# Performance work log

Measured on AMD Instinct MI355X. Metric: run time of the kernel, lower is better.

The kernel has to match this reference:

```python
import jax, jax.numpy as jnp
import numpy as np

GRID_SIZE = 8
IN_DIM = 1024
OUT_DIM = 1024
BATCH = 4096


def setup_inputs() -> dict:
    key = jax.random.key(0)
    k1, k2, k3 = jax.random.split(key, 3)
    noise_scale = 0.1
    noise_scale_base = 0.1
    x = jax.random.normal(k1, (BATCH, IN_DIM), dtype=jnp.float32)
    scale_base = (1.0 / np.sqrt(IN_DIM)
                  + (jax.random.normal(k2, (OUT_DIM, IN_DIM), dtype=jnp.float32) * 2 - 1)
                  * noise_scale_base)
    scale_spline = jnp.full((OUT_DIM, IN_DIM), 1.0, dtype=jnp.float32)
    coeff = (jax.random.uniform(k3, (2, OUT_DIM, IN_DIM, GRID_SIZE), dtype=jnp.float32)
             * noise_scale / (np.sqrt(IN_DIM) * np.sqrt(GRID_SIZE)))
    return {"x": x, "scale_base": scale_base, "scale_spline": scale_spline,
            "coeff": coeff}


def reference(x, scale_base, scale_spline, coeff):
    # x: (B, I); scale_base/scale_spline: (O, I); coeff: (2, O, I, G)
    G = coeff.shape[-1]
    k = jnp.arange(1, G + 1, dtype=x.dtype)          # (G,)
    ang = x[:, :, None] * k                           # (B, I, G)
    cos_b = jnp.cos(ang)
    sin_b = jnp.sin(ang)
    # fold scale_spline into coeff: (2, O, I, G)
    w = scale_spline[None, :, :, None] * coeff
    spline = (jnp.einsum('big,oig->bo', cos_b, w[0])
              + jnp.einsum('big,oig->bo', sin_b, w[1]))  # (B, O)
    base = jnp.einsum('bi,oi->bo', jax.nn.silu(x), scale_base)
    return base + spline
```

## Files before the change

### kernel.cpp

```cpp
#include <hip/hip_runtime.h>
#include <hip/hip_bf16.h>
#include <stdint.h>

#define BATCH   4096
#define IN_DIM  1024
#define OUT_DIM 1024
#define GRID_G  8
#define K8      16384
#define KB      1024
#define SPLITK  2
#define WSCALE  256.0f

typedef __bf16 bf16x8 __attribute__((ext_vector_type(8)));
typedef __bf16 bf16x4 __attribute__((ext_vector_type(4)));
typedef float  f32x4  __attribute__((ext_vector_type(4)));
typedef int    i32x4  __attribute__((ext_vector_type(4)));
typedef int    i32x8  __attribute__((ext_vector_type(8)));

__global__ __launch_bounds__(256) void prep(const float* __restrict__ x,
                                            const float* __restrict__ sb,
                                            const float* __restrict__ ss,
                                            const float* __restrict__ coeff,
                                            uint8_t* __restrict__ A8,
                                            uint8_t* __restrict__ W8,
                                            __bf16* __restrict__ Ab,
                                            __bf16* __restrict__ Wb,
                                            float* __restrict__ C) {
    __shared__ __align__(16) float lds[8192];
    const int tid = threadIdx.x;

    if (blockIdx.x < 1024) {
        const int t  = blockIdx.x * 256 + tid;
        const int b  = t >> 6;
        const int i0 = (t & 63) * 16;

        {
            float4 z = make_float4(0.f, 0.f, 0.f, 0.f);
            float4* cz = (float4*)(C + (size_t)blockIdx.x * 4096);
#pragma unroll
            for (int j = 0; j < 4; ++j) cz[j * 256 + tid] = z;
        }

        float xv[16];
        {
            const f32x4* xp = (const f32x4*)(x + (size_t)b * IN_DIM + i0);
            f32x4 q0 = __builtin_nontemporal_load(xp + 0);
            f32x4 q1 = __builtin_nontemporal_load(xp + 1);
            f32x4 q2 = __builtin_nontemporal_load(xp + 2);
            f32x4 q3 = __builtin_nontemporal_load(xp + 3);
#pragma unroll
            for (int j = 0; j < 4; ++j) {
                xv[j]      = q0[j];
                xv[4 + j]  = q1[j];
                xv[8 + j]  = q2[j];
                xv[12 + j] = q3[j];
            }
        }

        float c1[16], s1[16], ck[16], sk[16];
        bf16x8 va, vb;
#pragma unroll
        for (int j = 0; j < 16; ++j) {
            float e  = __expf(-xv[j]);
            float sl = xv[j] * __builtin_amdgcn_rcpf(1.f + e);
            if (j < 8) va[j & 7] = (__bf16)sl; else vb[j & 7] = (__bf16)sl;
            s1[j] = __sinf(xv[j]);
            c1[j] = __cosf(xv[j]);
            ck[j] = c1[j]; sk[j] = s1[j];
        }
        __builtin_nontemporal_store(va, (bf16x8*)(Ab + (size_t)b * IN_DIM + i0));
        __builtin_nontemporal_store(vb, (bf16x8*)(Ab + (size_t)b * IN_DIM + i0 + 8));

        uint8_t* a8 = A8 + (size_t)b * K8 + i0;
#pragma unroll
        for (int g = 0; g < GRID_G; ++g) {
            i32x4 wc, ws;
#pragma unroll
            for (int q = 0; q < 4; ++q) {
                int dc = 0, ds = 0;
                dc = __builtin_amdgcn_cvt_pk_fp8_f32(ck[4*q+0], ck[4*q+1], dc, false);
                dc = __builtin_amdgcn_cvt_pk_fp8_f32(ck[4*q+2], ck[4*q+3], dc, true);
                ds = __builtin_amdgcn_cvt_pk_fp8_f32(sk[4*q+0], sk[4*q+1], ds, false);
                ds = __builtin_amdgcn_cvt_pk_fp8_f32(sk[4*q+2], sk[4*q+3], ds, true);
                wc[q] = dc; ws[q] = ds;
            }
            __builtin_nontemporal_store(wc, (i32x4*)(a8 + (size_t)g * IN_DIM));
            __builtin_nontemporal_store(ws, (i32x4*)(a8 + (size_t)(GRID_G + g) * IN_DIM));
            if (g < GRID_G - 1) {
#pragma unroll
                for (int j = 0; j < 16; ++j) {
                    float cn = ck[j] * c1[j] - sk[j] * s1[j];
                    float sn = sk[j] * c1[j] + ck[j] * s1[j];
                    ck[j] = cn; sk[j] = sn;
                }
            }
        }
    } else {
        const int o   = blockIdx.x - 1024;
        const int i0  = tid * 4;
        const size_t oi = (size_t)o * IN_DIM + i0;

        const f32x4 s4 = __builtin_nontemporal_load((const f32x4*)(ss + oi));
        const float  s[4] = {s4[0] * WSCALE, s4[1] * WSCALE, s4[2] * WSCALE, s4[3] * WSCALE};

        {
            f32x4 b4 = __builtin_nontemporal_load((const f32x4*)(sb + oi));
            bf16x4 wv;
            wv[0] = (__bf16)b4[0]; wv[1] = (__bf16)b4[1];
            wv[2] = (__bf16)b4[2]; wv[3] = (__bf16)b4[3];
            __builtin_nontemporal_store(wv, (bf16x4*)(Wb + oi));
        }

        uint8_t* w8 = W8 + (size_t)o * K8 + i0;
        for (int p = 0; p < 2; ++p) {
            if (p) __syncthreads();
            const f32x4* src = (const f32x4*)(coeff + ((size_t)p * OUT_DIM + o) * (IN_DIM * GRID_G));
#pragma unroll
            for (int j = 0; j < 8; ++j) {
                f32x4 v = __builtin_nontemporal_load(src + j * 256 + tid);
                const int L   = j * 4096 + tid * 16;
                const int row = L >> 7;
                const int ch  = (L >> 4) & 7;
                *(f32x4*)((uint8_t*)lds + row * 128 + ((ch ^ (row & 7)) << 4)) = v;
            }
            __syncthreads();
            float c[4][8];
            {
                const uint8_t* rp = (const uint8_t*)lds + tid * 128;
                const int r7 = (tid & 7) << 4;
#pragma unroll
                for (int j = 0; j < 8; ++j) {
                    f32x4 v = *(const f32x4*)(rp + ((j << 4) ^ r7));
                    c[j >> 1][(j & 1) * 4 + 0] = v[0];
                    c[j >> 1][(j & 1) * 4 + 1] = v[1];
                    c[j >> 1][(j & 1) * 4 + 2] = v[2];
                    c[j >> 1][(j & 1) * 4 + 3] = v[3];
                }
            }
#pragma unroll
            for (int g = 0; g < GRID_G; ++g) {
                int d = 0;
                d = __builtin_amdgcn_cvt_pk_fp8_f32(s[0]*c[0][g], s[1]*c[1][g], d, false);
                d = __builtin_amdgcn_cvt_pk_fp8_f32(s[2]*c[2][g], s[3]*c[3][g], d, true);
                __builtin_nontemporal_store(d, (int*)(w8 + (size_t)(p * GRID_G + g) * IN_DIM));
            }
        }
    }
}

__global__ __launch_bounds__(256, 2) void gemm_all(const uint8_t* __restrict__ A8,
                                                   const uint8_t* __restrict__ W8,
                                                   const uint8_t* __restrict__ Ab,
                                                   const uint8_t* __restrict__ Wb,
                                                   float* __restrict__ C) {
    __shared__ __align__(16) uint8_t As[2][16384];
    __shared__ __align__(16) uint8_t Bs[2][16384];
    const int tid = threadIdx.x;
    const int w   = tid >> 6;
    const int l   = tid & 63;
    const int flat = blockIdx.y * 8 + blockIdx.x;
    const int xcd  = flat & 7;
    const int idx  = flat >> 3;
    const int bn   = (xcd & 1) * 4 + (idx & 3);
    const int bm   = (xcd >> 1) * 8 + (idx >> 2);
    const int kz  = blockIdx.z;
    const int wm  = w & 1;
    const int wn  = w >> 1;

    f32x4 acc[4][4] = {};

    const int srow   = l >> 3;
    const int schunk = ((l & 7) ^ srow) * 16;
    const int lm = l & 15;
    const int q  = l >> 4;
    const int c0 = (q * 2) << 4, c1 = (q * 2 + 1) << 4;

    {
        const uint8_t* Ag = A8 + (size_t)(bm * 128 + w * 32 + srow) * K8 + kz * (K8 / SPLITK) + schunk;
        const uint8_t* Bg = W8 + (size_t)(bn * 128 + w * 32 + srow) * K8 + kz * (K8 / SPLITK) + schunk;

        auto stage = [&](int bb) {
#pragma unroll
            for (int j = 0; j < 4; ++j) {
                __builtin_amdgcn_global_load_lds(
                    (const uint32_t*)(Ag + (size_t)(j * 8) * K8),
                    (uint32_t*)(&As[bb][(w * 32 + j * 8) * 128]), 16, 0, 0);
                __builtin_amdgcn_global_load_lds(
                    (const uint32_t*)(Bg + (size_t)(j * 8) * K8),
                    (uint32_t*)(&Bs[bb][(w * 32 + j * 8) * 128]), 16, 0, 0);
            }
            Ag += 128; Bg += 128;
        };
        auto compute = [&](int bb) {
            i32x8 bf[4];
#pragma unroll
            for (int j = 0; j < 4; ++j) {
                const int row = wn * 64 + j * 16 + lm;
                const int sw  = (row & 7) << 4;
                const uint8_t* rp = &Bs[bb][row * 128];
                i32x4 lo = *(const i32x4*)(rp + (c0 ^ sw));
                i32x4 hi = *(const i32x4*)(rp + (c1 ^ sw));
                bf[j] = __builtin_shufflevector(lo, hi, 0, 1, 2, 3, 4, 5, 6, 7);
            }
#pragma unroll
            for (int i = 0; i < 4; ++i) {
                const int row = wm * 64 + i * 16 + lm;
                const int sw  = (row & 7) << 4;
                const uint8_t* rp = &As[bb][row * 128];
                i32x4 lo = *(const i32x4*)(rp + (c0 ^ sw));
                i32x4 hi = *(const i32x4*)(rp + (c1 ^ sw));
                i32x8 af = __builtin_shufflevector(lo, hi, 0, 1, 2, 3, 4, 5, 6, 7);
#pragma unroll
                for (int j = 0; j < 4; ++j)
                    acc[i][j] = __builtin_amdgcn_mfma_scale_f32_16x16x128_f8f6f4(
                        af, bf[j], acc[i][j], 0, 0, 0, 0x7f7f7f7f, 0, 0x7f7f7f7f);
            }
        };

        stage(0);
        __syncthreads();
        for (int ks = 0; ks < 32; ++ks) {
            stage(1);
            compute(0);
            __syncthreads();
            if (ks < 31) stage(0);
            compute(1);
            __syncthreads();
        }
    }

#pragma unroll
    for (int i = 0; i < 4; ++i)
#pragma unroll
        for (int j = 0; j < 4; ++j)
            acc[i][j] *= (1.0f / WSCALE);

    {
        const uint8_t* Ag = Ab + (size_t)(bm * 128 + w * 32 + srow) * (KB * 2) + kz * (KB * 2 / SPLITK) + schunk;
        const uint8_t* Bg = Wb + (size_t)(bn * 128 + w * 32 + srow) * (KB * 2) + kz * (KB * 2 / SPLITK) + schunk;

        auto stage = [&](int bb) {
#pragma unroll
            for (int j = 0; j < 4; ++j) {
                __builtin_amdgcn_global_load_lds(
                    (const uint32_t*)(Ag + (size_t)(j * 8) * (KB * 2)),
                    (uint32_t*)(&As[bb][(w * 32 + j * 8) * 128]), 16, 0, 0);
                __builtin_amdgcn_global_load_lds(
                    (const uint32_t*)(Bg + (size_t)(j * 8) * (KB * 2)),
                    (uint32_t*)(&Bs[bb][(w * 32 + j * 8) * 128]), 16, 0, 0);
            }
            Ag += 128; Bg += 128;
        };
        auto compute = [&](int bb) {
#pragma unroll
            for (int h = 0; h < 2; ++h) {
                bf16x8 af[4], bfr[4];
#pragma unroll
                for (int i = 0; i < 4; ++i) {
                    const int row = wm * 64 + i * 16 + lm;
                    af[i] = *(const bf16x8*)(&As[bb][row * 128 + ((((h * 4 + q) ^ (row & 7))) << 4)]);
                }
#pragma unroll
                for (int j = 0; j < 4; ++j) {
                    const int row = wn * 64 + j * 16 + lm;
                    bfr[j] = *(const bf16x8*)(&Bs[bb][row * 128 + ((((h * 4 + q) ^ (row & 7))) << 4)]);
                }
#pragma unroll
                for (int i = 0; i < 4; ++i)
#pragma unroll
                    for (int j = 0; j < 4; ++j)
                        acc[i][j] = __builtin_amdgcn_mfma_f32_16x16x32_bf16(af[i], bfr[j], acc[i][j], 0, 0, 0);
            }
        };

        stage(0);
        __syncthreads();
        for (int kb = 0; kb < 4; ++kb) {
            stage(1);
            compute(0);
            __syncthreads();
            if (kb < 3) stage(0);
            compute(1);
            __syncthreads();
        }
    }

    const int row0 = bm * 128 + wm * 64 + q * 4;
    const int col0 = bn * 128 + wn * 64 + lm;
#pragma unroll
    for (int i = 0; i < 4; ++i)
#pragma unroll
        for (int j = 0; j < 4; ++j)
#pragma unroll
            for (int r = 0; r < 4; ++r)
                unsafeAtomicAdd(&C[(size_t)(row0 + i * 16 + r) * OUT_DIM + col0 + j * 16],
                                acc[i][j][r]);
}

extern "C" void kernel_launch(void* const* d_in, const int* in_sizes, int n_in,
                              void* d_out, int out_size, void* d_ws, size_t ws_size,
                              hipStream_t stream) {
    const float* x     = (const float*)d_in[0];
    const float* sb    = (const float*)d_in[1];
    const float* ss    = (const float*)d_in[2];
    const float* coeff = (const float*)d_in[3];
    float* out = (float*)d_out;

    uint8_t* A8 = (uint8_t*)d_ws;
    uint8_t* W8 = A8 + (size_t)BATCH * K8;
    __bf16*  Ab = (__bf16*)(W8 + (size_t)OUT_DIM * K8);
    __bf16*  Wb = Ab + (size_t)BATCH * KB;

    hipLaunchKernelGGL(prep, dim3(2048), dim3(256), 0, stream,
                       x, sb, ss, coeff, A8, W8, Ab, Wb, out);
    hipLaunchKernelGGL(gemm_all, dim3(OUT_DIM / 128, BATCH / 128, SPLITK), dim3(256), 0, stream,
                       A8, W8, (const uint8_t*)Ab, (const uint8_t*)Wb, out);
}
```

Before: 263.3 us.

## Prefetch two stages ahead with partial vmcnt waits in both GEMM loops

Both K-loops now issue the first two LDS stages before the loop. Each iteration waits only until the older stage's global_load_lds operations have landed (vmcnt(8)) rather than draining all loads, then refills the buffer it just consumed. The aim is to keep one stage of global loads in flight while the MFMAs run, instead of stalling on a full __syncthreads drain each half-iteration. This depends on the vmcnt count matching exactly 8 outstanding loads per stage. A wrong count, or compiler-inserted loads, would cause an LDS data race.

```diff
diff --git a/kernel.cpp b/kernel.cpp
--- a/kernel.cpp
+++ b/kernel.cpp
@@ -218,14 +218,16 @@
         };
 
         stage(0);
-        __syncthreads();
-        for (int ks = 0; ks < 32; ++ks) {
-            stage(1);
-            compute(0);
-            __syncthreads();
-            if (ks < 31) stage(0);
-            compute(1);
-            __syncthreads();
+        stage(1);
+        const int NT = (K8 / SPLITK) / 128;
+        for (int t = 0; t < NT; ++t) {
+            if (t < NT - 1) { asm volatile("s_waitcnt vmcnt(8)" ::: "memory"); }
+            else            { asm volatile("s_waitcnt vmcnt(0)" ::: "memory"); }
+            __builtin_amdgcn_sched_barrier(0);
+            __builtin_amdgcn_s_barrier();
+            compute(t & 1);
+            __builtin_amdgcn_s_barrier();
+            if (t < NT - 2) stage(t & 1);
         }
     }
 
@@ -274,14 +276,16 @@
         };
 
         stage(0);
-        __syncthreads();
-        for (int kb = 0; kb < 4; ++kb) {
-            stage(1);
-            compute(0);
-            __syncthreads();
-            if (kb < 3) stage(0);
-            compute(1);
-            __syncthreads();
+        stage(1);
+        const int NT = (KB * 2 / SPLITK) / 128;
+        for (int t = 0; t < NT; ++t) {
+            if (t < NT - 1) { asm volatile("s_waitcnt vmcnt(8)" ::: "memory"); }
+            else            { asm volatile("s_waitcnt vmcnt(0)" ::: "memory"); }
+            __builtin_amdgcn_sched_barrier(0);
+            __builtin_amdgcn_s_barrier();
+            compute(t & 1);
+            __builtin_amdgcn_s_barrier();
+            if (t < NT - 2) stage(t & 1);
         }
     }
 
```

Measured after the change: 243.2 us. 1.08x faster.
